# Optimization experiments

Measured on AMD Instinct MI355X. Metric: run time of the kernel, lower is better.

Reference implementation:

```python
import jax, jax.numpy as jnp
import numpy as np

B, T, DIM, HEADS = 8, 2048, 1024, 16
HD = DIM // HEADS


def setup_inputs() -> dict:
    key = jax.random.key(0)
    ks = jax.random.split(key, 12)
    s = 0.02
    z = jnp.zeros((DIM,), jnp.float32)
    return {
        "x": jax.random.normal(ks[0], (B, T, DIM), jnp.float32),
        "Wq": jax.random.normal(ks[1], (DIM, DIM), jnp.float32) * s,
        "bq": z,
        "Wk": jax.random.normal(ks[2], (DIM, DIM), jnp.float32) * s,
        "bk": z,
        "Wv": jax.random.normal(ks[3], (DIM, DIM), jnp.float32) * s,
        "bv": z,
        "w_rwkv": jax.random.normal(ks[4], (HEADS, HD), jnp.float32) * 0.5,
        "u_rwkv": jax.random.normal(ks[5], (HEADS, HD), jnp.float32) * 0.5,
        "Wo": jax.random.normal(ks[6], (DIM, DIM), jnp.float32) * s,
        "bo": z,
    }


def reference(x, Wq, bq, Wk, bk, Wv, bv, w_rwkv, u_rwkv, Wo, bo):
    N, T_, _ = x.shape
    # queries are computed but never used in the original forward
    _ = x @ Wq + bq
    k = (x @ Wk + bk).reshape(N, T_, HEADS, HD)
    v = (x @ Wv + bv).reshape(N, T_, HEADS, HD)
    kt = jnp.moveaxis(k, 1, 0)  # [T, N, H, D]
    vt = jnp.moveaxis(v, 1, 0)  # [T, N, H, D]

    u = u_rwkv  # [H, D] broadcasts against [N, H, D]
    w = w_rwkv

    def step(carry, kv):
        pp, aa, bb = carry
        k_t, v_t = kv
        # output at step t (with bonus u)
        ww = u + k_t
        qq = jnp.maximum(ww, pp)
        e1 = jnp.exp(pp - qq)
        e2 = jnp.exp(ww - qq)
        o_t = (e1 * aa + e2 * v_t) / (e1 * bb + e2)
        # state update (with decay w)
        ww2 = pp - w
        qq2 = jnp.maximum(ww2, k_t)
        e1b = jnp.exp(ww2 - qq2)
        e2b = jnp.exp(k_t - qq2)
        aa2 = e1b * aa + e2b * v_t
        bb2 = e1b * bb + e2b
        return (qq2, aa2, bb2), o_t

    init = (kt[0], vt[0], jnp.ones_like(kt[0]))  # pp, aa, bb
    _, o_rest = jax.lax.scan(step, init, (kt[1:], vt[1:]))  # [T-1, N, H, D]
    O = jnp.concatenate([vt[:1], o_rest], axis=0)  # O[0] = v[0]
    O = jnp.moveaxis(O, 0, 1).reshape(N, T_, -1)  # [N, T, dim]
    return O @ Wo + bo
```

## Files before the change

kernel.cpp:

```cpp
#include <hip/hip_runtime.h>

#define DIMSZ 1024
#define NB 8
#define TSEQ 2048
#define MTOT (NB*TSEQ)
#define CCH 64
#define LCH (TSEQ/CCH)
#define NCHAN (NB*DIMSZ)

typedef __attribute__((ext_vector_type(8))) short short8v;
typedef __attribute__((ext_vector_type(4))) float f32x4;

__device__ __forceinline__ unsigned short f2bf(float f) {
  unsigned int u; __builtin_memcpy(&u, &f, 4);
  unsigned int r = u + 0x7FFF + ((u >> 16) & 1);
  return (unsigned short)(r >> 16);
}
__device__ __forceinline__ float bf2f(unsigned short us) {
  unsigned int v = ((unsigned int)us) << 16;
  float f; __builtin_memcpy(&f, &v, 4); return f;
}

__device__ __forceinline__ void gload16(const void* g, void* l) {
  __builtin_amdgcn_global_load_lds(
      (const __attribute__((address_space(1))) void*)g,
      (__attribute__((address_space(3))) void*)l, 16, 0, 0);
}

__global__ __launch_bounds__(256) void cast_x_kernel(
    const float* __restrict__ in, unsigned short* __restrict__ out) {
  int i = blockIdx.x * 256 + threadIdx.x;
  float4 f = reinterpret_cast<const float4*>(in)[i];
  uint2 o;
  o.x = (unsigned)f2bf(f.x) | ((unsigned)f2bf(f.y) << 16);
  o.y = (unsigned)f2bf(f.z) | ((unsigned)f2bf(f.w) << 16);
  reinterpret_cast<uint2*>(out)[i] = o;
}

__global__ __launch_bounds__(256) void transpose_cast_kernel(
    const float* __restrict__ W, unsigned short* __restrict__ WT) {
  __shared__ float tile[32][33];
  int tx = threadIdx.x & 31, ty = threadIdx.x >> 5;
  int row0 = blockIdx.y * 32, col0 = blockIdx.x * 32;
  #pragma unroll
  for (int j = 0; j < 32; j += 8)
    tile[ty + j][tx] = W[(size_t)(row0 + ty + j) * DIMSZ + col0 + tx];
  __syncthreads();
  #pragma unroll
  for (int j = 0; j < 32; j += 8)
    WT[(size_t)(col0 + ty + j) * DIMSZ + row0 + tx] = f2bf(tile[tx][ty + j]);
}


#define VM6 asm volatile("s_waitcnt vmcnt(6)" ::: "memory")
#define VM0 asm volatile("s_waitcnt vmcnt(0)" ::: "memory")

#define PH_BAR do {                         \
  __builtin_amdgcn_s_barrier();             \
  __builtin_amdgcn_sched_barrier(0);        \
} while(0)

#define STAGE(BUF, OP, HALF, T) do {                                        \
  const unsigned short* _s = (OP) ? BT : Aop;                               \
  const int _rb = ((OP) ? bcol : brow) + (HALF)*128 + wid*16;               \
  char* _lb = smem + (BUF)*65536 + (OP)*32768 + ((HALF)*128 + wid*16)*128;  \
  const size_t _k0 = (size_t)(T)*64;                                        \
  gload16(&_s[(size_t)(_rb + srow)*K + _k0 + (sg^srow)*8], _lb);            \
  gload16(&_s[(size_t)(_rb + 8 + srow)*K + _k0 + (sg^srow)*8], _lb + 1024); \
} while(0)

#define READ_A(DST, BUF, MH) do {                                           \
  _Pragma("unroll")                                                         \
  for (int _m = 0; _m < 4; ++_m) {                                          \
    const char* _pa = smem + (BUF)*65536 +                                  \
        ((MH)*128 + wr*64 + _m*16 + lrow)*128;                              \
    DST[_m][0] = *(const short8v*)(_pa + ((lko*2) ^ rds));                  \
    DST[_m][1] = *(const short8v*)(_pa + (((32+lko)*2) ^ rds));             \
  }                                                                         \
} while(0)

#define READ_B(DST, BUF, NH) do {                                           \
  _Pragma("unroll")                                                         \
  for (int _n = 0; _n < 2; ++_n) {                                          \
    const char* _pb = smem + (BUF)*65536 + 32768 +                          \
        ((NH)*128 + wc*32 + _n*16 + lrow)*128;                              \
    DST[_n][0] = *(const short8v*)(_pb + ((lko*2) ^ rds));                  \
    DST[_n][1] = *(const short8v*)(_pb + (((32+lko)*2) ^ rds));             \
  }                                                                         \
} while(0)

#define MFMA_Q(MH, NH, AF, BF) do {                                         \
  __builtin_amdgcn_s_setprio(1);                                            \
  _Pragma("unroll")                                                         \
  for (int _m = 0; _m < 4; ++_m)                                            \
    _Pragma("unroll")                                                       \
    for (int _n = 0; _n < 2; ++_n) {                                        \
      acc[(MH)*4+_m][(NH)*2+_n] = __builtin_amdgcn_mfma_f32_16x16x32_bf16(  \
          AF[_m][0], BF[_n][0], acc[(MH)*4+_m][(NH)*2+_n], 0, 0, 0);        \
      acc[(MH)*4+_m][(NH)*2+_n] = __builtin_amdgcn_mfma_f32_16x16x32_bf16(  \
          AF[_m][1], BF[_n][1], acc[(MH)*4+_m][(NH)*2+_n], 0, 0, 0);        \
    }                                                                       \
  __builtin_amdgcn_s_setprio(0);                                            \
} while(0)

template<int OUTBF>
__global__ __launch_bounds__(512) void gemm256_kernel(
    const unsigned short* __restrict__ Aop,
    const unsigned short* __restrict__ BT,
    void* __restrict__ Cv,
    const float* __restrict__ bias0,
    const float* __restrict__ bias1,
    int M, int N, int K, int Nsplit) {
  extern __shared__ char smem[];
  const int tid  = threadIdx.x;
  const int wid  = tid >> 6;
  const int lane = tid & 63;
  const int wr   = wid >> 2;
  const int wc   = wid & 3;
  const int brow = blockIdx.x * 256;
  const int bcol = blockIdx.y * 256;
  const int lrow = lane & 15;
  const int lko  = (lane >> 4) * 8;
  const int rds  = (lrow & 7) << 4;
  const int srow = lane >> 3;
  const int sg   = lane & 7;

  f32x4 acc[8][4];
  #pragma unroll
  for (int m = 0; m < 8; ++m)
    #pragma unroll
    for (int n = 0; n < 4; ++n)
      acc[m][n] = (f32x4){0.f, 0.f, 0.f, 0.f};

  short8v a0[4][2], a1[4][2], bf0[2][2], bf1[2][2];

  STAGE(0, 0, 0, 0); STAGE(0, 1, 0, 0); STAGE(0, 1, 1, 0); STAGE(0, 0, 1, 0);
  STAGE(1, 0, 0, 1); STAGE(1, 1, 0, 1); STAGE(1, 1, 1, 1);
  VM6;
  PH_BAR;

  const int NT = K >> 6;
  for (int t = 0; t < NT; ++t) {
    const int b = t & 1, nb = b ^ 1;
    const bool s1 = (t + 1 < NT), s2 = (t + 2 < NT);
    READ_A(a0, b, 0); READ_B(bf0, b, 0);
    if (s1) STAGE(nb, 0, 1, t + 1);
    PH_BAR;
    MFMA_Q(0, 0, a0, bf0); PH_BAR;
    READ_B(bf1, b, 1);
    if (s2) STAGE(b, 0, 0, t + 2);
    PH_BAR;
    MFMA_Q(0, 1, a0, bf1); PH_BAR;
    READ_A(a1, b, 1);
    if (s2) STAGE(b, 1, 0, t + 2);
    PH_BAR;
    MFMA_Q(1, 0, a1, bf0); PH_BAR;
    if (s2) { STAGE(b, 1, 1, t + 2); VM6; }
    else if (s1) { VM0; }
    PH_BAR;
    MFMA_Q(1, 1, a1, bf1); PH_BAR;
  }

  #pragma unroll
  for (int mf = 0; mf < 8; ++mf) {
    const int rowb = brow + (mf >= 4) * 128 + wr * 64 + (mf & 3) * 16 + (lane >> 4) * 4;
    #pragma unroll
    for (int nf = 0; nf < 4; ++nf) {
      const int col = bcol + (nf >= 2) * 128 + wc * 32 + (nf & 1) * 16 + lrow;
      const float bb = (col < Nsplit) ? bias0[col] : bias1[col - Nsplit];
      #pragma unroll
      for (int r = 0; r < 4; ++r) {
        const float val = acc[mf][nf][r] + bb;
        if (OUTBF) {
          ((unsigned short*)Cv)[(size_t)(rowb + r) * N + col] = f2bf(val);
        } else {
          ((float*)Cv)[(size_t)(rowb + r) * N + col] = val;
        }
      }
    }
  }
}


__device__ __forceinline__ void wkv_step(float& p, float& a, float& b,
                                         float kt, float vt, float w) {
  float ww2 = p - w;
  float qq2 = fmaxf(ww2, kt);
  float e1 = __expf(ww2 - qq2);
  float e2 = __expf(kt - qq2);
  a = e1 * a + e2 * vt;
  b = e1 * b + e2;
  p = qq2;
}

__global__ __launch_bounds__(256) void wkv_chunk_state_kernel(
    const unsigned short* __restrict__ kv,
    const float* __restrict__ wdec,
    float* __restrict__ stP, float* __restrict__ stA, float* __restrict__ stB) {
  int idx = blockIdx.x * 256 + threadIdx.x;
  int cp = idx & 511;
  int n = (idx >> 9) & (NB - 1);
  int chunk = idx >> 12;
  int c = cp * 2;
  float2 w2 = *reinterpret_cast<const float2*>(&wdec[c]);
  const unsigned short* base = kv + (size_t)(n * TSEQ + chunk * LCH) * 2048 + c;
  float p0 = -1e30f, a0 = 0.f, b0 = 0.f;
  float p1 = -1e30f, a1 = 0.f, b1 = 0.f;
  #pragma unroll 8
  for (int j = 0; j < LCH; ++j) {
    unsigned int kk = *reinterpret_cast<const unsigned int*>(&base[(size_t)j * 2048]);
    unsigned int vv = *reinterpret_cast<const unsigned int*>(&base[(size_t)j * 2048 + 1024]);
    wkv_step(p0, a0, b0, bf2f(kk & 0xffff), bf2f(vv & 0xffff), w2.x);
    wkv_step(p1, a1, b1, bf2f(kk >> 16),    bf2f(vv >> 16),    w2.y);
  }
  int soff = chunk * NCHAN + n * 1024 + c;
  *reinterpret_cast<float2*>(&stP[soff]) = make_float2(p0, p1);
  *reinterpret_cast<float2*>(&stA[soff]) = make_float2(a0, a1);
  *reinterpret_cast<float2*>(&stB[soff]) = make_float2(b0, b1);
}

__global__ __launch_bounds__(256) void wkv_scan_kernel(
    const float* __restrict__ wdec,
    float* __restrict__ stP, float* __restrict__ stA, float* __restrict__ stB) {
  int idx = blockIdx.x * 256 + threadIdx.x;
  int c = idx & 1023;
  float decay = (float)LCH * wdec[c];
  float p = -1e30f, a = 0.f, b = 0.f;
  for (int i = 0; i < CCH; ++i) {
    int off = i * NCHAN + idx;
    float pc = stP[off], ac = stA[off], bc = stB[off];
    stP[off] = p; stA[off] = a; stB[off] = b;
    float pd = p - decay;
    float q = fmaxf(pd, pc);
    float e1 = __expf(pd - q);
    float e2 = __expf(pc - q);
    a = e1 * a + e2 * ac;
    b = e1 * b + e2 * bc;
    p = q;
  }
}

__global__ __launch_bounds__(256) void wkv_out_kernel(
    const unsigned short* __restrict__ kv,
    const float* __restrict__ wdec, const float* __restrict__ ubon,
    const float* __restrict__ stP, const float* __restrict__ stA,
    const float* __restrict__ stB,
    unsigned short* __restrict__ O) {
  int idx = blockIdx.x * 256 + threadIdx.x;
  int cp = idx & 511;
  int n = (idx >> 9) & (NB - 1);
  int chunk = idx >> 12;
  int c = cp * 2;
  float2 w2 = *reinterpret_cast<const float2*>(&wdec[c]);
  float2 u2 = *reinterpret_cast<const float2*>(&ubon[c]);
  const unsigned short* base = kv + (size_t)(n * TSEQ + chunk * LCH) * 2048 + c;
  unsigned short* ob = O + (size_t)(n * TSEQ + chunk * LCH) * DIMSZ + c;
  int soff = chunk * NCHAN + n * 1024 + c;
  float2 pP = *reinterpret_cast<const float2*>(&stP[soff]);
  float2 pA = *reinterpret_cast<const float2*>(&stA[soff]);
  float2 pB = *reinterpret_cast<const float2*>(&stB[soff]);
  float p0 = pP.x, a0 = pA.x, b0 = pB.x;
  float p1 = pP.y, a1 = pA.y, b1 = pB.y;
  #pragma unroll 4
  for (int j = 0; j < LCH; ++j) {
    unsigned int kk = *reinterpret_cast<const unsigned int*>(&base[(size_t)j * 2048]);
    unsigned int vv = *reinterpret_cast<const unsigned int*>(&base[(size_t)j * 2048 + 1024]);
    float k0 = bf2f(kk & 0xffff), k1 = bf2f(kk >> 16);
    float v0 = bf2f(vv & 0xffff), v1 = bf2f(vv >> 16);
    float ww0 = u2.x + k0, ww1 = u2.y + k1;
    float qq0 = fmaxf(ww0, p0), qq1 = fmaxf(ww1, p1);
    float e10 = __expf(p0 - qq0), e20 = __expf(ww0 - qq0);
    float e11 = __expf(p1 - qq1), e21 = __expf(ww1 - qq1);
    float o0 = (e10 * a0 + e20 * v0) * __builtin_amdgcn_rcpf(e10 * b0 + e20);
    float o1 = (e11 * a1 + e21 * v1) * __builtin_amdgcn_rcpf(e11 * b1 + e21);
    *reinterpret_cast<unsigned int*>(&ob[(size_t)j * DIMSZ]) =
        (unsigned)f2bf(o0) | ((unsigned)f2bf(o1) << 16);
    wkv_step(p0, a0, b0, k0, v0, w2.x);
    wkv_step(p1, a1, b1, k1, v1, w2.y);
  }
}

extern "C" void kernel_launch(void* const* d_in, const int* in_sizes, int n_in,
                              void* d_out, int out_size, void* d_ws, size_t ws_size,
                              hipStream_t stream) {
  const float* x  = (const float*)d_in[0];
  const float* Wk = (const float*)d_in[3];
  const float* bk = (const float*)d_in[4];
  const float* Wv = (const float*)d_in[5];
  const float* bv = (const float*)d_in[6];
  const float* wr = (const float*)d_in[7];
  const float* ur = (const float*)d_in[8];
  const float* Wo = (const float*)d_in[9];
  const float* bo = (const float*)d_in[10];
  float* out = (float*)d_out;

  char* ws = (char*)d_ws;
  unsigned short* xb   = (unsigned short*)(ws);
  unsigned short* WTkv = (unsigned short*)(ws + 33554432);
  unsigned short* WoT  = (unsigned short*)(ws + 37748736);
  unsigned short* kvb  = (unsigned short*)(ws + 39845888);

  float* stP = out;
  float* stA = out + CCH * NCHAN;
  float* stB = out + 2 * CCH * NCHAN;

  cast_x_kernel<<<dim3(16384), dim3(256), 0, stream>>>(x, xb);
  transpose_cast_kernel<<<dim3(32, 32), dim3(256), 0, stream>>>(Wk, WTkv);
  transpose_cast_kernel<<<dim3(32, 32), dim3(256), 0, stream>>>(Wv, WTkv + 1024 * 1024);
  transpose_cast_kernel<<<dim3(32, 32), dim3(256), 0, stream>>>(Wo, WoT);

  gemm256_kernel<1><<<dim3(64, 8), dim3(512), 131072, stream>>>(
      xb, WTkv, (void*)kvb, bk, bv, MTOT, 2048, 1024, 1024);

  wkv_chunk_state_kernel<<<dim3(CCH * NB * 512 / 256), dim3(256), 0, stream>>>(
      kvb, wr, stP, stA, stB);
  wkv_scan_kernel<<<dim3(NCHAN / 256), dim3(256), 0, stream>>>(wr, stP, stA, stB);
  wkv_out_kernel<<<dim3(CCH * NB * 512 / 256), dim3(256), 0, stream>>>(
      kvb, wr, ur, stP, stA, stB, xb);

  gemm256_kernel<0><<<dim3(64, 4), dim3(512), 131072, stream>>>(
      xb, WoT, (void*)out, bo, bo, MTOT, 1024, 1024, 1024);
}
```

Measured before the change: 174.7 us.

## Restructure GEMM LDS layout and prefetch schedule; widen WKV kernels to four channels

The GEMM main loop is rewritten so each tile stages the whole next K-tile into the alternate buffer and preloads the first A/B fragments for the next iteration. The LDS layout is rearranged so fragment reads become fixed base pointers plus constant offsets, and the wait count changes from vmcnt(6) to vmcnt(2). The intent is to cut address arithmetic and overlap global loads with the MFMA phases better. Separately, the WKV chunk-state and output kernels now process four channels per thread with 8-byte loads and stores, halving the thread count, which trades parallelism for wider memory accesses and more independent work per thread.

```diff
diff --git a/kernel.cpp b/kernel.cpp
--- a/kernel.cpp
+++ b/kernel.cpp
@@ -52,7 +52,7 @@
 }
 
 
-#define VM6 asm volatile("s_waitcnt vmcnt(6)" ::: "memory")
+#define VM2 asm volatile("s_waitcnt vmcnt(2)" ::: "memory")
 #define VM0 asm volatile("s_waitcnt vmcnt(0)" ::: "memory")
 
 #define PH_BAR do {                         \
@@ -63,29 +63,27 @@
 #define STAGE(BUF, OP, HALF, T) do {                                        \
   const unsigned short* _s = (OP) ? BT : Aop;                               \
   const int _rb = ((OP) ? bcol : brow) + (HALF)*128 + wid*16;               \
-  char* _lb = smem + (BUF)*65536 + (OP)*32768 + ((HALF)*128 + wid*16)*128;  \
+  char* _lb = smem + (OP)*65536 + (BUF)*32768 + (HALF)*16384 + wid*2048;    \
   const size_t _k0 = (size_t)(T)*64;                                        \
   gload16(&_s[(size_t)(_rb + srow)*K + _k0 + (sg^srow)*8], _lb);            \
   gload16(&_s[(size_t)(_rb + 8 + srow)*K + _k0 + (sg^srow)*8], _lb + 1024); \
 } while(0)
 
+#define RD16(P, OFF) (*(const short8v*)((P) + (OFF)))
+
 #define READ_A(DST, BUF, MH) do {                                           \
   _Pragma("unroll")                                                         \
   for (int _m = 0; _m < 4; ++_m) {                                          \
-    const char* _pa = smem + (BUF)*65536 +                                  \
-        ((MH)*128 + wr*64 + _m*16 + lrow)*128;                              \
-    DST[_m][0] = *(const short8v*)(_pa + ((lko*2) ^ rds));                  \
-    DST[_m][1] = *(const short8v*)(_pa + (((32+lko)*2) ^ rds));             \
+    DST[_m][0] = RD16(pA0, (BUF)*32768 + (MH)*16384 + _m*2048);             \
+    DST[_m][1] = RD16(pA1, (BUF)*32768 + (MH)*16384 + _m*2048);             \
   }                                                                         \
 } while(0)
 
 #define READ_B(DST, BUF, NH) do {                                           \
   _Pragma("unroll")                                                         \
   for (int _n = 0; _n < 2; ++_n) {                                          \
-    const char* _pb = smem + (BUF)*65536 + 32768 +                          \
-        ((NH)*128 + wc*32 + _n*16 + lrow)*128;                              \
-    DST[_n][0] = *(const short8v*)(_pb + ((lko*2) ^ rds));                  \
-    DST[_n][1] = *(const short8v*)(_pb + (((32+lko)*2) ^ rds));             \
+    DST[_n][0] = RD16(pB0, (BUF)*32768 + (NH)*16384 + _n*2048);             \
+    DST[_n][1] = RD16(pB1, (BUF)*32768 + (NH)*16384 + _n*2048);             \
   }                                                                         \
 } while(0)
 
@@ -101,6 +99,31 @@
           AF[_m][1], BF[_n][1], acc[(MH)*4+_m][(NH)*2+_n], 0, 0, 0);        \
     }                                                                       \
   __builtin_amdgcn_s_setprio(0);                                            \
+} while(0)
+
+#define TILE(B_, NB_, T) do {                                               \
+  const int _t = (T);                                                       \
+  const bool s1 = (_t + 1 < NT);                                            \
+                                                                   \
+  READ_B(bf1, B_, 1);                                                       \
+  if (s1) STAGE(NB_, 0, 0, _t + 1);                                         \
+  if (s1) { VM2; } else { VM0; }                        \
+  PH_BAR;                                                                   \
+  MFMA_Q(0, 0, a0, bf0); PH_BAR;                                            \
+                                                                   \
+  READ_A(a1, B_, 1);                                                        \
+  if (s1) STAGE(NB_, 1, 0, _t + 1);                                         \
+  PH_BAR;                                                                   \
+  MFMA_Q(0, 1, a0, bf1); PH_BAR;                                            \
+                                                                   \
+  if (s1) STAGE(NB_, 1, 1, _t + 1);                                         \
+  PH_BAR;                                                                   \
+  MFMA_Q(1, 0, a1, bf0); PH_BAR;                                            \
+     \
+  if (s1) { STAGE(NB_, 0, 1, _t + 1); VM2; }                                \
+  PH_BAR;                                                                   \
+  if (s1) { READ_A(a0, NB_, 0); READ_B(bf0, NB_, 0); }                      \
+  MFMA_Q(1, 1, a1, bf1); PH_BAR;                                            \
 } while(0)
 
 template<int OUTBF>
@@ -125,6 +148,11 @@
   const int srow = lane >> 3;
   const int sg   = lane & 7;
 
+  const char* pA0 = smem + (wr*64 + lrow)*128 + ((lko*2) ^ rds);
+  const char* pA1 = smem + (wr*64 + lrow)*128 + ((64 + lko*2) ^ rds);
+  const char* pB0 = smem + 65536 + (wc*32 + lrow)*128 + ((lko*2) ^ rds);
+  const char* pB1 = smem + 65536 + (wc*32 + lrow)*128 + ((64 + lko*2) ^ rds);
+
   f32x4 acc[8][4];
   #pragma unroll
   for (int m = 0; m < 8; ++m)
@@ -135,30 +163,14 @@
   short8v a0[4][2], a1[4][2], bf0[2][2], bf1[2][2];
 
   STAGE(0, 0, 0, 0); STAGE(0, 1, 0, 0); STAGE(0, 1, 1, 0); STAGE(0, 0, 1, 0);
-  STAGE(1, 0, 0, 1); STAGE(1, 1, 0, 1); STAGE(1, 1, 1, 1);
-  VM6;
+  VM2;
   PH_BAR;
+  READ_A(a0, 0, 0); READ_B(bf0, 0, 0);
 
   const int NT = K >> 6;
-  for (int t = 0; t < NT; ++t) {
-    const int b = t & 1, nb = b ^ 1;
-    const bool s1 = (t + 1 < NT), s2 = (t + 2 < NT);
-    READ_A(a0, b, 0); READ_B(bf0, b, 0);
-    if (s1) STAGE(nb, 0, 1, t + 1);
-    PH_BAR;
-    MFMA_Q(0, 0, a0, bf0); PH_BAR;
-    READ_B(bf1, b, 1);
-    if (s2) STAGE(b, 0, 0, t + 2);
-    PH_BAR;
-    MFMA_Q(0, 1, a0, bf1); PH_BAR;
-    READ_A(a1, b, 1);
-    if (s2) STAGE(b, 1, 0, t + 2);
-    PH_BAR;
-    MFMA_Q(1, 0, a1, bf0); PH_BAR;
-    if (s2) { STAGE(b, 1, 1, t + 2); VM6; }
-    else if (s1) { VM0; }
-    PH_BAR;
-    MFMA_Q(1, 1, a1, bf1); PH_BAR;
+  for (int t = 0; t < NT; t += 2) {
+    TILE(0, 1, t);
+    TILE(1, 0, t + 1);
   }
 
   #pragma unroll
@@ -198,25 +210,27 @@
     const float* __restrict__ wdec,
     float* __restrict__ stP, float* __restrict__ stA, float* __restrict__ stB) {
   int idx = blockIdx.x * 256 + threadIdx.x;
-  int cp = idx & 511;
-  int n = (idx >> 9) & (NB - 1);
-  int chunk = idx >> 12;
-  int c = cp * 2;
-  float2 w2 = *reinterpret_cast<const float2*>(&wdec[c]);
+  int cq = idx & 255;
+  int n = (idx >> 8) & (NB - 1);
+  int chunk = idx >> 11;
+  int c = cq * 4;
+  float4 w4 = *reinterpret_cast<const float4*>(&wdec[c]);
   const unsigned short* base = kv + (size_t)(n * TSEQ + chunk * LCH) * 2048 + c;
-  float p0 = -1e30f, a0 = 0.f, b0 = 0.f;
-  float p1 = -1e30f, a1 = 0.f, b1 = 0.f;
+  float p0=-1e30f,a0=0.f,b0=0.f, p1=-1e30f,a1=0.f,b1=0.f;
+  float p2=-1e30f,a2=0.f,b2=0.f, p3=-1e30f,a3=0.f,b3=0.f;
   #pragma unroll 8
   for (int j = 0; j < LCH; ++j) {
-    unsigned int kk = *reinterpret_cast<const unsigned int*>(&base[(size_t)j * 2048]);
-    unsigned int vv = *reinterpret_cast<const unsigned int*>(&base[(size_t)j * 2048 + 1024]);
-    wkv_step(p0, a0, b0, bf2f(kk & 0xffff), bf2f(vv & 0xffff), w2.x);
-    wkv_step(p1, a1, b1, bf2f(kk >> 16),    bf2f(vv >> 16),    w2.y);
+    uint2 kk = *reinterpret_cast<const uint2*>(&base[(size_t)j * 2048]);
+    uint2 vv = *reinterpret_cast<const uint2*>(&base[(size_t)j * 2048 + 1024]);
+    wkv_step(p0,a0,b0, bf2f(kk.x & 0xffff), bf2f(vv.x & 0xffff), w4.x);
+    wkv_step(p1,a1,b1, bf2f(kk.x >> 16),    bf2f(vv.x >> 16),    w4.y);
+    wkv_step(p2,a2,b2, bf2f(kk.y & 0xffff), bf2f(vv.y & 0xffff), w4.z);
+    wkv_step(p3,a3,b3, bf2f(kk.y >> 16),    bf2f(vv.y >> 16),    w4.w);
   }
   int soff = chunk * NCHAN + n * 1024 + c;
-  *reinterpret_cast<float2*>(&stP[soff]) = make_float2(p0, p1);
-  *reinterpret_cast<float2*>(&stA[soff]) = make_float2(a0, a1);
-  *reinterpret_cast<float2*>(&stB[soff]) = make_float2(b0, b1);
+  *reinterpret_cast<float4*>(&stP[soff]) = make_float4(p0, p1, p2, p3);
+  *reinterpret_cast<float4*>(&stA[soff]) = make_float4(a0, a1, a2, a3);
+  *reinterpret_cast<float4*>(&stB[soff]) = make_float4(b0, b1, b2, b3);
 }
 
 __global__ __launch_bounds__(256) void wkv_scan_kernel(
@@ -247,36 +261,46 @@
     const float* __restrict__ stB,
     unsigned short* __restrict__ O) {
   int idx = blockIdx.x * 256 + threadIdx.x;
-  int cp = idx & 511;
-  int n = (idx >> 9) & (NB - 1);
-  int chunk = idx >> 12;
-  int c = cp * 2;
-  float2 w2 = *reinterpret_cast<const float2*>(&wdec[c]);
-  float2 u2 = *reinterpret_cast<const float2*>(&ubon[c]);
+  int cq = idx & 255;
+  int n = (idx >> 8) & (NB - 1);
+  int chunk = idx >> 11;
+  int c = cq * 4;
+  float4 w4 = *reinterpret_cast<const float4*>(&wdec[c]);
+  float4 u4 = *reinterpret_cast<const float4*>(&ubon[c]);
   const unsigned short* base = kv + (size_t)(n * TSEQ + chunk * LCH) * 2048 + c;
   unsigned short* ob = O + (size_t)(n * TSEQ + chunk * LCH) * DIMSZ + c;
   int soff = chunk * NCHAN + n * 1024 + c;
-  float2 pP = *reinterpret_cast<const float2*>(&stP[soff]);
-  float2 pA = *reinterpret_cast<const float2*>(&stA[soff]);
-  float2 pB = *reinterpret_cast<const float2*>(&stB[soff]);
-  float p0 = pP.x, a0 = pA.x, b0 = pB.x;
-  float p1 = pP.y, a1 = pA.y, b1 = pB.y;
+  float4 pP = *reinterpret_cast<const float4*>(&stP[soff]);
+  float4 pA = *reinterpret_cast<const float4*>(&stA[soff]);
+  float4 pB = *reinterpret_cast<const float4*>(&stB[soff]);
+  float p0=pP.x,a0=pA.x,b0=pB.x, p1=pP.y,a1=pA.y,b1=pB.y;
+  float p2=pP.z,a2=pA.z,b2=pB.z, p3=pP.w,a3=pA.w,b3=pB.w;
   #pragma unroll 4
   for (int j = 0; j < LCH; ++j) {
-    unsigned int kk = *reinterpret_cast<const unsigned int*>(&base[(size_t)j * 2048]);
-    unsigned int vv = *reinterpret_cast<const unsigned int*>(&base[(size_t)j * 2048 + 1024]);
-    float k0 = bf2f(kk & 0xffff), k1 = bf2f(kk >> 16);
-    float v0 = bf2f(vv & 0xffff), v1 = bf2f(vv >> 16);
-    float ww0 = u2.x + k0, ww1 = u2.y + k1;
-    float qq0 = fmaxf(ww0, p0), qq1 = fmaxf(ww1, p1);
-    float e10 = __expf(p0 - qq0), e20 = __expf(ww0 - qq0);
-    float e11 = __expf(p1 - qq1), e21 = __expf(ww1 - qq1);
-    float o0 = (e10 * a0 + e20 * v0) * __builtin_amdgcn_rcpf(e10 * b0 + e20);
-    float o1 = (e11 * a1 + e21 * v1) * __builtin_amdgcn_rcpf(e11 * b1 + e21);
-    *reinterpret_cast<unsigned int*>(&ob[(size_t)j * DIMSZ]) =
-        (unsigned)f2bf(o0) | ((unsigned)f2bf(o1) << 16);
-    wkv_step(p0, a0, b0, k0, v0, w2.x);
-    wkv_step(p1, a1, b1, k1, v1, w2.y);
+    uint2 kk = *reinterpret_cast<const uint2*>(&base[(size_t)j * 2048]);
+    uint2 vv = *reinterpret_cast<const uint2*>(&base[(size_t)j * 2048 + 1024]);
+    float k0 = bf2f(kk.x & 0xffff), k1 = bf2f(kk.x >> 16);
+    float k2 = bf2f(kk.y & 0xffff), k3 = bf2f(kk.y >> 16);
+    float v0 = bf2f(vv.x & 0xffff), v1 = bf2f(vv.x >> 16);
+    float v2 = bf2f(vv.y & 0xffff), v3 = bf2f(vv.y >> 16);
+    float ww0=u4.x+k0, ww1=u4.y+k1, ww2=u4.z+k2, ww3=u4.w+k3;
+    float qq0=fmaxf(ww0,p0), qq1=fmaxf(ww1,p1), qq2=fmaxf(ww2,p2), qq3=fmaxf(ww3,p3);
+    float e10=__expf(p0-qq0), e20=__expf(ww0-qq0);
+    float e11=__expf(p1-qq1), e21=__expf(ww1-qq1);
+    float e12=__expf(p2-qq2), e22=__expf(ww2-qq2);
+    float e13=__expf(p3-qq3), e23=__expf(ww3-qq3);
+    float o0=(e10*a0+e20*v0)*__builtin_amdgcn_rcpf(e10*b0+e20);
+    float o1=(e11*a1+e21*v1)*__builtin_amdgcn_rcpf(e11*b1+e21);
+    float o2=(e12*a2+e22*v2)*__builtin_amdgcn_rcpf(e12*b2+e22);
+    float o3=(e13*a3+e23*v3)*__builtin_amdgcn_rcpf(e13*b3+e23);
+    uint2 ow;
+    ow.x = (unsigned)f2bf(o0) | ((unsigned)f2bf(o1) << 16);
+    ow.y = (unsigned)f2bf(o2) | ((unsigned)f2bf(o3) << 16);
+    *reinterpret_cast<uint2*>(&ob[(size_t)j * DIMSZ]) = ow;
+    wkv_step(p0,a0,b0,k0,v0,w4.x);
+    wkv_step(p1,a1,b1,k1,v1,w4.y);
+    wkv_step(p2,a2,b2,k2,v2,w4.z);
+    wkv_step(p3,a3,b3,k3,v3,w4.w);
   }
 }
 
@@ -312,10 +336,10 @@
   gemm256_kernel<1><<<dim3(64, 8), dim3(512), 131072, stream>>>(
       xb, WTkv, (void*)kvb, bk, bv, MTOT, 2048, 1024, 1024);
 
-  wkv_chunk_state_kernel<<<dim3(CCH * NB * 512 / 256), dim3(256), 0, stream>>>(
+  wkv_chunk_state_kernel<<<dim3(CCH * NB), dim3(256), 0, stream>>>(
       kvb, wr, stP, stA, stB);
   wkv_scan_kernel<<<dim3(NCHAN / 256), dim3(256), 0, stream>>>(wr, stP, stA, stB);
-  wkv_out_kernel<<<dim3(CCH * NB * 512 / 256), dim3(256), 0, stream>>>(
+  wkv_out_kernel<<<dim3(CCH * NB), dim3(256), 0, stream>>>(
       kvb, wr, ur, stP, stA, stB, xb);
 
   gemm256_kernel<0><<<dim3(64, 4), dim3(512), 131072, stream>>>(
```

Result: no change. 175.1 us (+0.3%).
